# Optimization experiments

Measured on AMD Instinct MI355X. Metric: run time of the kernel, lower is better.

The kernel has to match this reference:

```python
import jax, jax.numpy as jnp
import numpy as np
from math import sqrt

B, T, C, H = 4, 2048, 1024, 16
D = C // H  # head dim = 64


def setup_inputs() -> dict:
    key = jax.random.key(0)
    ks = jax.random.split(key, 9)
    s = 1.0 / sqrt(C)
    return {
        "x": jax.random.normal(ks[0], (B, T, C), dtype=jnp.float32),
        "Wk": jax.random.normal(ks[1], (C, C), dtype=jnp.float32) * s,
        "bk": jax.random.normal(ks[2], (C,), dtype=jnp.float32) * 0.01,
        "Wq": jax.random.normal(ks[3], (C, C), dtype=jnp.float32) * s,
        "bq": jax.random.normal(ks[4], (C,), dtype=jnp.float32) * 0.01,
        "Wv": jax.random.normal(ks[5], (C, C), dtype=jnp.float32) * s,
        "bv": jax.random.normal(ks[6], (C,), dtype=jnp.float32) * 0.01,
        "Wp": jax.random.normal(ks[7], (C, C), dtype=jnp.float32) * s,
        "bp": jax.random.normal(ks[8], (C,), dtype=jnp.float32) * 0.01,
    }


def reference(x, Wk, bk, Wq, bq, Wv, bv, Wp, bp):
    # Linear projections, split into heads: [B, H, T, D]
    def heads(y):
        return y.reshape(B, T, H, D).transpose(0, 2, 1, 3)

    k = heads(x @ Wk + bk)
    q = heads(x @ Wq + bq)
    v = heads(x @ Wv + bv)

    # scaled dot-product attention with causal mask (dropout p=0 -> identity)
    attn = jnp.einsum("bhtd,bhsd->bhts", q, k) / jnp.sqrt(jnp.float32(D))
    causal = jnp.tril(jnp.ones((T, T), dtype=bool))
    attn = jnp.where(causal[None, None], attn, -jnp.inf)
    attn = jax.nn.softmax(attn, axis=-1)

    y = jnp.einsum("bhts,bhsd->bhtd", attn, v)  # [B, H, T, D]
    y = y.transpose(0, 2, 1, 3).reshape(B, T, C)
    return y @ Wp + bp
```

## Files before the change

kernel.cpp:

```cpp
#include <hip/hip_runtime.h>
#include <hip/hip_bf16.h>
#include <math.h>


typedef short bf16x8 __attribute__((ext_vector_type(8)));
typedef float f32x4 __attribute__((ext_vector_type(4)));
typedef _Float16 f16x4 __attribute__((ext_vector_type(4)));

__device__ __forceinline__ short f2b(float f) {
    unsigned u = __float_as_uint(f);
    u = (u + 0x7fffu + ((u >> 16) & 1u)) >> 16;
    return (short)u;
}
__device__ __forceinline__ float b2f(short s) {
    return __uint_as_float(((unsigned)(unsigned short)s) << 16);
}

__global__ __launch_bounds__(256) void cast_x_kernel(const float* __restrict__ x,
                                                     short* __restrict__ xb, int n4) {
    int idx = blockIdx.x * 256 + threadIdx.x;
    if (idx >= n4) return;
    float4 v = ((const float4*)x)[idx];
    short4 o;
    o.x = f2b(v.x); o.y = f2b(v.y); o.z = f2b(v.z); o.w = f2b(v.w);
    ((short4*)xb)[idx] = o;
}

__global__ __launch_bounds__(256) void wtrans_kernel(const float* W0, const float* W1,
                                                     const float* W2, const float* W3,
                                                     short* O0, short* O1, short* O2, short* O3) {
    const float* W; short* O;
    switch (blockIdx.z) {
        case 0: W = W0; O = O0; break;
        case 1: W = W1; O = O1; break;
        case 2: W = W2; O = O2; break;
        default: W = W3; O = O3; break;
    }
    __shared__ __align__(16) float Ls[64 * 68];
    int tid = threadIdx.x;
    int n0 = blockIdx.x * 64, k0 = blockIdx.y * 64;
    #pragma unroll
    for (int it = 0; it < 4; ++it) {
        int c = tid + it * 256;
        int r = c >> 4, off = (c & 15) * 4;
        *(float4*)&Ls[r * 68 + off] = *(const float4*)&W[(k0 + r) * 1024 + n0 + off];
    }
    __syncthreads();
    #pragma unroll
    for (int it = 0; it < 2; ++it) {
        int c = tid + it * 256;
        int n = c >> 3, koff = (c & 7) * 8;
        union { short s[8]; int4 v; } u;
        #pragma unroll
        for (int k = 0; k < 8; ++k) u.s[k] = f2b(Ls[(koff + k) * 68 + n]);
        *(int4*)&O[(n0 + n) * 1024 + k0 + koff] = u.v;
    }
}

template<int MODE>
__global__ __launch_bounds__(256) void gemm_kernel(const short* __restrict__ A,
                                                   const short* Bt0, const short* Bt1, const short* Bt2,
                                                   const float* b0, const float* b1, const float* b2,
                                                   float s0, float s1, float s2,
                                                   void* O0, void* O1, void* O2) {
    int z = blockIdx.z;
    const short* Bt   = (z == 0) ? Bt0 : (z == 1) ? Bt1 : Bt2;
    const float* bias = (z == 0) ? b0  : (z == 1) ? b1  : b2;
    float scl         = (z == 0) ? s0  : (z == 1) ? s1  : s2;
    void* Out         = (z == 0) ? O0  : (z == 1) ? O1  : O2;

    __shared__ __align__(16) short As[128 * 64];
    __shared__ __align__(16) short Bs[128 * 64];

    int tid = threadIdx.x;
    int w = tid >> 6, lane = tid & 63, quad = lane >> 4, l15 = lane & 15;
    int m0 = blockIdx.x * 128, n0 = blockIdx.y * 128;
    int wm = (w >> 1) * 64, wn = (w & 1) * 64;
    int lrow = lane >> 3, lcol = (lane & 7) * 8;

    f32x4 acc[4][4] = {};

    for (int kt = 0; kt < 16; ++kt) {
        int k0 = kt * 64;
        __syncthreads();
        #pragma unroll
        for (int it = 0; it < 4; ++it) {
            int r0 = it * 32 + w * 8;
            __builtin_amdgcn_global_load_lds(
                (const __attribute__((address_space(1))) unsigned int*)&A[(m0 + r0 + lrow) * 1024 + k0 + lcol],
                (__attribute__((address_space(3))) unsigned int*)&As[r0 * 64], 16, 0, 0);
            __builtin_amdgcn_global_load_lds(
                (const __attribute__((address_space(1))) unsigned int*)&Bt[(n0 + r0 + lrow) * 1024 + k0 + lcol],
                (__attribute__((address_space(3))) unsigned int*)&Bs[r0 * 64], 16, 0, 0);
        }
        __syncthreads();
        #pragma unroll
        for (int kk = 0; kk < 2; ++kk) {
            bf16x8 af[4], bf[4];
            #pragma unroll
            for (int i = 0; i < 4; ++i)
                af[i] = *(const bf16x8*)&As[(wm + i * 16 + l15) * 64 + kk * 32 + quad * 8];
            #pragma unroll
            for (int j = 0; j < 4; ++j)
                bf[j] = *(const bf16x8*)&Bs[(wn + j * 16 + l15) * 64 + kk * 32 + quad * 8];
            #pragma unroll
            for (int i = 0; i < 4; ++i)
                #pragma unroll
                for (int j = 0; j < 4; ++j)
                    acc[i][j] = __builtin_amdgcn_mfma_f32_16x16x32_bf16(af[i], bf[j], acc[i][j], 0, 0, 0);
        }
    }
    #pragma unroll
    for (int i = 0; i < 4; ++i) {
        #pragma unroll
        for (int j = 0; j < 4; ++j) {
            int gn = n0 + wn + j * 16 + l15;
            float bv = bias[gn];
            #pragma unroll
            for (int r = 0; r < 4; ++r) {
                int gm = m0 + wm + i * 16 + quad * 4 + r;
                float v = (acc[i][j][r] + bv) * scl;
                if (MODE == 0) {
                    int b = gm >> 11, t = gm & 2047, h = gn >> 6, d = gn & 63;
                    ((short*)Out)[(((b * 16 + h) * 2048) + t) * 64 + d] = f2b(v);
                } else {
                    ((float*)Out)[gm * 1024 + gn] = v;
                }
            }
        }
    }
}

__global__ __launch_bounds__(256) void vtrans_kernel(const short* __restrict__ V,
                                                     _Float16* __restrict__ Vt) {
    __shared__ __align__(16) short Ts[64 * 72];
    int tid = threadIdx.x;
    int bh = blockIdx.y;
    int t0 = blockIdx.x * 64;
    #pragma unroll
    for (int it = 0; it < 2; ++it) {
        int c = tid + it * 256;
        int r = c >> 3, off = (c & 7) * 8;
        *(int4*)&Ts[r * 72 + off] = *(const int4*)&V[(bh * 2048 + t0 + r) * 64 + off];
    }
    __syncthreads();
    #pragma unroll
    for (int it = 0; it < 2; ++it) {
        int c = tid + it * 256;
        int d = c >> 3, toff = (c & 7) * 8;
        union { _Float16 h[8]; int4 v; } u;
        #pragma unroll
        for (int k = 0; k < 8; ++k) u.h[k] = (_Float16)b2f(Ts[(toff + k) * 72 + d]);
        *(int4*)&Vt[(bh * 64 + d) * 2048 + t0 + toff] = u.v;
    }
}

__global__ __launch_bounds__(256, 3) void attn_kernel(const short* __restrict__ Q,
                                                      const short* __restrict__ K,
                                                      const _Float16* __restrict__ Vt,
                                                      short* __restrict__ Y) {
    __shared__ __align__(16) short    Ks[128 * 64];
    __shared__ __align__(16) _Float16 Vs[64 * 128];

    int tid = threadIdx.x;
    int w = tid >> 6, lane = tid & 63, quad = lane >> 4, l15 = lane & 15;
    int idx = blockIdx.x;
    int qi = 15 - (idx >> 6);
    int bh = idx & 63;

    const short* Qh = Q + bh * 2048 * 64;
    const short* Kh = K + bh * 2048 * 64;
    const _Float16* Vh = Vt + bh * 64 * 2048;

    bf16x8 qf[2][2];
    #pragma unroll
    for (int i = 0; i < 2; ++i)
        #pragma unroll
        for (int kh = 0; kh < 2; ++kh) {
            int t = qi * 128 + w * 32 + i * 16 + l15;
            qf[i][kh] = *(const bf16x8*)&Qh[t * 64 + kh * 32 + quad * 8];
        }

    int krow = lane >> 3;
    int kchunk = ((lane & 7) ^ krow) * 8;
    int vrow = lane >> 4;
    int vchunk = ((lane & 15) ^ (w * 4 + vrow)) * 8;

    int t7 = l15 & 7;
    int kf0_off = ((quad ^ t7) * 8);
    int kf1_off = (((quad + 4) ^ t7) * 8);
    int vsub = (quad & 1) * 4;
    int vchi = quad >> 1;

    f32x4 o[2][4] = {};
    float lsum[2] = {0.f, 0.f};

    for (int si = 0; si <= qi; ++si) {
        const short* Kt = Kh + si * 128 * 64;
        const _Float16* Vtile = Vh + si * 128;
        bool diag = (si == qi);

        __syncthreads();
        #pragma unroll
        for (int it = 0; it < 4; ++it) {
            int kr0 = it * 32 + w * 8;
            __builtin_amdgcn_global_load_lds(
                (const __attribute__((address_space(1))) unsigned int*)&Kt[(kr0 + krow) * 64 + kchunk],
                (__attribute__((address_space(3))) unsigned int*)&Ks[kr0 * 64], 16, 0, 0);
            int vr0 = it * 16 + w * 4;
            __builtin_amdgcn_global_load_lds(
                (const __attribute__((address_space(1))) unsigned int*)&Vtile[(vr0 + vrow) * 2048 + vchunk],
                (__attribute__((address_space(3))) unsigned int*)&Vs[vr0 * 128], 16, 0, 0);
        }
        __syncthreads();

        #pragma unroll
        for (int j = 0; j < 8; ++j) {
            int trow = (j * 16 + l15) * 64;
            bf16x8 kf0 = *(const bf16x8*)&Ks[trow + kf0_off];
            bf16x8 kf1 = *(const bf16x8*)&Ks[trow + kf1_off];
            f16x4 pfv[2];
            #pragma unroll
            for (int i = 0; i < 2; ++i) {
                f32x4 a = {};
                a = __builtin_amdgcn_mfma_f32_16x16x32_bf16(kf0, qf[i][0], a, 0, 0, 0);
                a = __builtin_amdgcn_mfma_f32_16x16x32_bf16(kf1, qf[i][1], a, 0, 0, 0);
                if (diag) {
                    int qrel = w * 32 + i * 16 + l15;
                    #pragma unroll
                    for (int r = 0; r < 4; ++r)
                        if (j * 16 + quad * 4 + r > qrel) a[r] = -1e30f;
                }
                float p0 = __builtin_amdgcn_exp2f(a[0]);
                float p1 = __builtin_amdgcn_exp2f(a[1]);
                float p2 = __builtin_amdgcn_exp2f(a[2]);
                float p3 = __builtin_amdgcn_exp2f(a[3]);
                lsum[i] += (p0 + p1) + (p2 + p3);
                pfv[i][0] = (_Float16)p0;
                pfv[i][1] = (_Float16)p1;
                pfv[i][2] = (_Float16)p2;
                pfv[i][3] = (_Float16)p3;
            }
            int vc = (j * 2 + vchi);
            #pragma unroll
            for (int mt = 0; mt < 4; ++mt) {
                int d = mt * 16 + l15;
                f16x4 vf = *(const f16x4*)&Vs[d * 128 + ((vc ^ l15) * 8) + vsub];
                o[0][mt] = __builtin_amdgcn_mfma_f32_16x16x16f16(vf, pfv[0], o[0][mt], 0, 0, 0);
                o[1][mt] = __builtin_amdgcn_mfma_f32_16x16x16f16(vf, pfv[1], o[1][mt], 0, 0, 0);
            }
        }
    }

    int b = bh >> 4, h = bh & 15;
    #pragma unroll
    for (int i = 0; i < 2; ++i) {
        float l = lsum[i];
        l += __shfl_xor(l, 16);
        l += __shfl_xor(l, 32);
        float rinv = 1.0f / l;
        int q = qi * 128 + w * 32 + i * 16 + l15;
        short* yrow = &Y[(b * 2048 + q) * 1024 + h * 64];
        #pragma unroll
        for (int mt = 0; mt < 4; ++mt) {
            short4 s4;
            s4.x = f2b(o[i][mt][0] * rinv);
            s4.y = f2b(o[i][mt][1] * rinv);
            s4.z = f2b(o[i][mt][2] * rinv);
            s4.w = f2b(o[i][mt][3] * rinv);
            *(short4*)&yrow[mt * 16 + quad * 4] = s4;
        }
    }
}

extern "C" void kernel_launch(void* const* d_in, const int* in_sizes, int n_in,
                              void* d_out, int out_size, void* d_ws, size_t ws_size,
                              hipStream_t stream) {
    const float* x  = (const float*)d_in[0];
    const float* Wk = (const float*)d_in[1];
    const float* bk = (const float*)d_in[2];
    const float* Wq = (const float*)d_in[3];
    const float* bq = (const float*)d_in[4];
    const float* Wv = (const float*)d_in[5];
    const float* bv = (const float*)d_in[6];
    const float* Wp = (const float*)d_in[7];
    const float* bp = (const float*)d_in[8];

    char* ws = (char*)d_ws;
    short*     xb  = (short*)(ws + 0);
    short*     Wqt = (short*)(ws + 16777216);
    short*     Wkt = (short*)(ws + 18874368);
    short*     Wvt = (short*)(ws + 20971520);
    short*     Wpt = (short*)(ws + 23068672);
    short*     Qb  = (short*)(ws + 25165824);
    short*     Kb  = (short*)(ws + 41943040);
    short*     Vb  = (short*)(ws + 58720256);
    _Float16*  Vtb = (_Float16*)(ws + 75497472);
    short*     Yb  = (short*)(ws + 92274688);

    cast_x_kernel<<<8192, 256, 0, stream>>>(x, xb, 2097152);
    wtrans_kernel<<<dim3(16, 16, 4), 256, 0, stream>>>(Wq, Wk, Wv, Wp, Wqt, Wkt, Wvt, Wpt);
    gemm_kernel<0><<<dim3(64, 8, 3), 256, 0, stream>>>(xb, Wqt, Wkt, Wvt, bq, bk, bv,
                                                       0.18033688011112042f , 1.0f, 1.0f,
                                                       (void*)Qb, (void*)Kb, (void*)Vb);
    vtrans_kernel<<<dim3(32, 64), 256, 0, stream>>>(Vb, Vtb);
    attn_kernel<<<1024, 256, 0, stream>>>(Qb, Kb, Vtb, Yb);
    gemm_kernel<1><<<dim3(64, 8, 1), 256, 0, stream>>>(Yb, Wpt, nullptr, nullptr,
                                                       bp, nullptr, nullptr,
                                                       1.0f, 1.0f, 1.0f,
                                                       (void*)d_out, nullptr, nullptr);
}
```

Measured before the change: 255.1 us.

## Rewrite projection GEMMs as 8-wave triple-buffered pipelined kernel with swizzled LDS

Replaces the 128x128, 4-wave GEMM with a 128x256 tile run by 8 waves. K-tiles are triple-buffered in LDS and staged with global_load_lds two steps ahead, using an XOR swizzle to avoid bank conflicts. The MFMA phases are split into two half-tiles, each with its own barrier and s_setprio, so global loads overlap with compute. This targets the memory-latency stalls of the old load-sync-compute loop. In exchange it uses a large LDS footprint (144KB), adds register pressure and launches fewer blocks.

```diff
diff --git a/kernel.cpp b/kernel.cpp
--- a/kernel.cpp
+++ b/kernel.cpp
@@ -58,73 +58,147 @@
 }
 
 template<int MODE>
-__global__ __launch_bounds__(256) void gemm_kernel(const short* __restrict__ A,
-                                                   const short* Bt0, const short* Bt1, const short* Bt2,
-                                                   const float* b0, const float* b1, const float* b2,
-                                                   float s0, float s1, float s2,
-                                                   void* O0, void* O1, void* O2) {
+__global__ __launch_bounds__(512, 2) void gemm8_kernel(const short* __restrict__ A,
+                                                       const short* Bt0, const short* Bt1, const short* Bt2,
+                                                       const float* b0, const float* b1, const float* b2,
+                                                       float s0, float s1, float s2,
+                                                       void* O0, void* O1, void* O2) {
     int z = blockIdx.z;
     const short* Bt   = (z == 0) ? Bt0 : (z == 1) ? Bt1 : Bt2;
     const float* bias = (z == 0) ? b0  : (z == 1) ? b1  : b2;
     float scl         = (z == 0) ? s0  : (z == 1) ? s1  : s2;
     void* Out         = (z == 0) ? O0  : (z == 1) ? O1  : O2;
 
-    __shared__ __align__(16) short As[128 * 64];
-    __shared__ __align__(16) short Bs[128 * 64];
+    __shared__ __align__(16) short lds[73728];
 
     int tid = threadIdx.x;
     int w = tid >> 6, lane = tid & 63, quad = lane >> 4, l15 = lane & 15;
-    int m0 = blockIdx.x * 128, n0 = blockIdx.y * 128;
-    int wm = (w >> 1) * 64, wn = (w & 1) * 64;
-    int lrow = lane >> 3, lcol = (lane & 7) * 8;
-
-    f32x4 acc[4][4] = {};
-
-    for (int kt = 0; kt < 16; ++kt) {
-        int k0 = kt * 64;
-        __syncthreads();
-        #pragma unroll
-        for (int it = 0; it < 4; ++it) {
-            int r0 = it * 32 + w * 8;
-            __builtin_amdgcn_global_load_lds(
-                (const __attribute__((address_space(1))) unsigned int*)&A[(m0 + r0 + lrow) * 1024 + k0 + lcol],
-                (__attribute__((address_space(3))) unsigned int*)&As[r0 * 64], 16, 0, 0);
-            __builtin_amdgcn_global_load_lds(
-                (const __attribute__((address_space(1))) unsigned int*)&Bt[(n0 + r0 + lrow) * 1024 + k0 + lcol],
-                (__attribute__((address_space(3))) unsigned int*)&Bs[r0 * 64], 16, 0, 0);
-        }
-        __syncthreads();
-        #pragma unroll
-        for (int kk = 0; kk < 2; ++kk) {
-            bf16x8 af[4], bf[4];
-            #pragma unroll
-            for (int i = 0; i < 4; ++i)
-                af[i] = *(const bf16x8*)&As[(wm + i * 16 + l15) * 64 + kk * 32 + quad * 8];
-            #pragma unroll
-            for (int j = 0; j < 4; ++j)
-                bf[j] = *(const bf16x8*)&Bs[(wn + j * 16 + l15) * 64 + kk * 32 + quad * 8];
-            #pragma unroll
-            for (int i = 0; i < 4; ++i)
+    int m0 = blockIdx.x * 128, n0 = blockIdx.y * 256;
+
+    int srccol = ((lane & 3) * 8) ^ ((lane & 32) ? 16 : 0);
+    const short* pA0 = A  + (m0 + w * 16 + (lane >> 2)) * 1024 + srccol;
+    const short* pA1 = pA0 + 32;
+    const short* pB0 = Bt + (n0 + (2 * w) * 16 + (lane >> 2)) * 1024 + srccol;
+    const short* pB1 = pB0 + 32;
+    const short* pB2 = pB0 + 16 * 1024;
+    const short* pB3 = pB2 + 32;
+
+    int dA = (w * 2) * 512;
+    int dB = 24576 + (w * 4) * 512;
+
+    int offR = l15 * 64 + ((quad * 16) ^ ((l15 & 8) << 2));
+    int ma4 = (w >> 2) * 4;
+    int nb2 = (w & 3) * 2;
+    const char* ldsb = (const char*)lds;
+
+    f32x4 acc[2][4][2] = {};
+
+#define STG(p, off) __builtin_amdgcn_global_load_lds( \
+        (const __attribute__((address_space(1))) unsigned int*)(p), \
+        (__attribute__((address_space(3))) unsigned int*)&lds[off], 16, 0, 0)
+
+    STG(pA0,      dA);                 STG(pA1,      dA + 512);
+    STG(pB0,      dB);                 STG(pB1,      dB + 512);
+    STG(pB2,      dB + 1024);          STG(pB3,      dB + 1536);
+    STG(pA0 + 64, 8192 + dA);          STG(pA1 + 64, 8192 + dA + 512);
+    STG(pB0 + 64, 16384 + dB);         STG(pB1 + 64, 16384 + dB + 512);
+    STG(pB2 + 64, 16384 + dB + 1024);  STG(pB3 + 64, 16384 + dB + 1536);
+    asm volatile("s_waitcnt vmcnt(6)" ::: "memory");
+    __builtin_amdgcn_s_barrier();
+    __builtin_amdgcn_sched_barrier(0);
+
+    #pragma unroll
+    for (int t = 0; t < 16; ++t) {
+        const int rs = t % 3;
+        const int ss = (t + 2) % 3;
+        const int Ar = rs * 16384;
+        const int Br = 49152 + rs * 32768;
+
+        bf16x8 af[4][2], bf[2][2];
+        #pragma unroll
+        for (int i = 0; i < 4; ++i)
+            #pragma unroll
+            for (int kk = 0; kk < 2; ++kk)
+                af[i][kk] = *(const bf16x8*)(ldsb + Ar + ((ma4 + i) * 2 + kk) * 1024 + offR);
+        #pragma unroll
+        for (int j = 0; j < 2; ++j)
+            #pragma unroll
+            for (int kk = 0; kk < 2; ++kk)
+                bf[j][kk] = *(const bf16x8*)(ldsb + Br + ((nb2 + j) * 2 + kk) * 1024 + offR);
+        if (t + 2 < 16) {
+            STG(pA0 + (t + 2) * 64, ss * 8192 + dA);
+            STG(pA1 + (t + 2) * 64, ss * 8192 + dA + 512);
+            STG(pB0 + (t + 2) * 64, ss * 16384 + dB);
+        }
+        __builtin_amdgcn_s_barrier();
+        asm volatile("s_waitcnt lgkmcnt(0)" ::: "memory");
+        __builtin_amdgcn_sched_barrier(0);
+        __builtin_amdgcn_s_setprio(1);
+        #pragma unroll
+        for (int i = 0; i < 4; ++i)
+            #pragma unroll
+            for (int j = 0; j < 2; ++j) {
+                acc[0][i][j] = __builtin_amdgcn_mfma_f32_16x16x32_bf16(af[i][0], bf[j][0], acc[0][i][j], 0, 0, 0);
+                acc[0][i][j] = __builtin_amdgcn_mfma_f32_16x16x32_bf16(af[i][1], bf[j][1], acc[0][i][j], 0, 0, 0);
+            }
+        __builtin_amdgcn_s_setprio(0);
+        __builtin_amdgcn_s_barrier();
+        __builtin_amdgcn_sched_barrier(0);
+
+        #pragma unroll
+        for (int j = 0; j < 2; ++j)
+            #pragma unroll
+            for (int kk = 0; kk < 2; ++kk)
+                bf[j][kk] = *(const bf16x8*)(ldsb + Br + ((8 + nb2 + j) * 2 + kk) * 1024 + offR);
+        if (t + 2 < 16) {
+            STG(pB1 + (t + 2) * 64, ss * 16384 + dB + 512);
+            STG(pB2 + (t + 2) * 64, ss * 16384 + dB + 1024);
+            STG(pB3 + (t + 2) * 64, ss * 16384 + dB + 1536);
+        }
+        __builtin_amdgcn_s_barrier();
+        asm volatile("s_waitcnt lgkmcnt(0)" ::: "memory");
+        __builtin_amdgcn_sched_barrier(0);
+        __builtin_amdgcn_s_setprio(1);
+        #pragma unroll
+        for (int i = 0; i < 4; ++i)
+            #pragma unroll
+            for (int j = 0; j < 2; ++j) {
+                acc[1][i][j] = __builtin_amdgcn_mfma_f32_16x16x32_bf16(af[i][0], bf[j][0], acc[1][i][j], 0, 0, 0);
+                acc[1][i][j] = __builtin_amdgcn_mfma_f32_16x16x32_bf16(af[i][1], bf[j][1], acc[1][i][j], 0, 0, 0);
+            }
+        __builtin_amdgcn_s_setprio(0);
+        if (t < 14) {
+            asm volatile("s_waitcnt vmcnt(6)" ::: "memory");
+        } else if (t == 14) {
+            asm volatile("s_waitcnt vmcnt(0)" ::: "memory");
+        }
+        if (t < 15) {
+            __builtin_amdgcn_s_barrier();
+            __builtin_amdgcn_sched_barrier(0);
+        }
+    }
+#undef STG
+
+    int mrow = m0 + (w >> 2) * 64;
+    int ncol = n0 + (w & 3) * 32;
+    #pragma unroll
+    for (int nh = 0; nh < 2; ++nh) {
+        #pragma unroll
+        for (int i = 0; i < 4; ++i) {
+            #pragma unroll
+            for (int j = 0; j < 2; ++j) {
+                int gn = ncol + nh * 128 + j * 16 + l15;
+                float bv = bias[gn];
                 #pragma unroll
-                for (int j = 0; j < 4; ++j)
-                    acc[i][j] = __builtin_amdgcn_mfma_f32_16x16x32_bf16(af[i], bf[j], acc[i][j], 0, 0, 0);
-        }
-    }
-    #pragma unroll
-    for (int i = 0; i < 4; ++i) {
-        #pragma unroll
-        for (int j = 0; j < 4; ++j) {
-            int gn = n0 + wn + j * 16 + l15;
-            float bv = bias[gn];
-            #pragma unroll
-            for (int r = 0; r < 4; ++r) {
-                int gm = m0 + wm + i * 16 + quad * 4 + r;
-                float v = (acc[i][j][r] + bv) * scl;
-                if (MODE == 0) {
-                    int b = gm >> 11, t = gm & 2047, h = gn >> 6, d = gn & 63;
-                    ((short*)Out)[(((b * 16 + h) * 2048) + t) * 64 + d] = f2b(v);
-                } else {
-                    ((float*)Out)[gm * 1024 + gn] = v;
+                for (int r = 0; r < 4; ++r) {
+                    int gm = mrow + i * 16 + quad * 4 + r;
+                    float v = (acc[nh][i][j][r] + bv) * scl;
+                    if (MODE == 0) {
+                        int b = gm >> 11, tt = gm & 2047, h = gn >> 6, d = gn & 63;
+                        ((short*)Out)[(((b * 16 + h) * 2048) + tt) * 64 + d] = f2b(v);
+                    } else {
+                        ((float*)Out)[gm * 1024 + gn] = v;
+                    }
                 }
             }
         }
@@ -300,13 +374,13 @@
 
     cast_x_kernel<<<8192, 256, 0, stream>>>(x, xb, 2097152);
     wtrans_kernel<<<dim3(16, 16, 4), 256, 0, stream>>>(Wq, Wk, Wv, Wp, Wqt, Wkt, Wvt, Wpt);
-    gemm_kernel<0><<<dim3(64, 8, 3), 256, 0, stream>>>(xb, Wqt, Wkt, Wvt, bq, bk, bv,
-                                                       0.18033688011112042f , 1.0f, 1.0f,
-                                                       (void*)Qb, (void*)Kb, (void*)Vb);
+    gemm8_kernel<0><<<dim3(64, 4, 3), 512, 0, stream>>>(xb, Wqt, Wkt, Wvt, bq, bk, bv,
+                                                        0.18033688011112042f , 1.0f, 1.0f,
+                                                        (void*)Qb, (void*)Kb, (void*)Vb);
     vtrans_kernel<<<dim3(32, 64), 256, 0, stream>>>(Vb, Vtb);
     attn_kernel<<<1024, 256, 0, stream>>>(Qb, Kb, Vtb, Yb);
-    gemm_kernel<1><<<dim3(64, 8, 1), 256, 0, stream>>>(Yb, Wpt, nullptr, nullptr,
-                                                       bp, nullptr, nullptr,
-                                                       1.0f, 1.0f, 1.0f,
-                                                       (void*)d_out, nullptr, nullptr);
-}
+    gemm8_kernel<1><<<dim3(64, 4, 1), 512, 0, stream>>>(Yb, Wpt, nullptr, nullptr,
+                                                        bp, nullptr, nullptr,
+                                                        1.0f, 1.0f, 1.0f,
+                                                        (void*)d_out, nullptr, nullptr);
+}
```

New measurement: 241.9 us. 5.2% less time.
